# Kernel tuning notes

Measured on AMD Instinct MI355X. Metric: run time of the kernel, lower is better.

Reference implementation:

```python
import jax, jax.numpy as jnp
import numpy as np
from jax import lax

STRIDES = [8, 16, 32, 64, 128]
NUM_CLASSES = 80
PRE_NMS_THRESH = 0.05
PRE_NMS_TOP_N = 1000
NMS_THRESH = 0.6
MAX_DET = 100
IMG_SIZE = 800.0
BBOX_W = (10.0, 10.0, 5.0, 5.0)
SCALE_CLAMP = float(np.log(1000.0 / 16.0))  # Box2BoxTransform clamp


def conv3x3(x, w, b):
    y = lax.conv_general_dilated(x, w, (1, 1), 'SAME',
                                 dimension_numbers=('NCHW', 'OIHW', 'NCHW'))
    return y + b[None, :, None, None]


def conv1x1(x, w, b):
    return jnp.einsum('nchw,kc->nkhw', x, w) + b[None, :, None, None]


def make_anchors(H, W, stride):
    # one square anchor per location, size = 8 * stride (ATSS), offset 0.5
    size = 8.0 * stride
    xs = (jnp.arange(W, dtype=jnp.float32) + 0.5) * stride
    ys = (jnp.arange(H, dtype=jnp.float32) + 0.5) * stride
    cy, cx = jnp.meshgrid(ys, xs, indexing='ij')
    half = size / 2.0
    return jnp.stack([cx - half, cy - half, cx + half, cy + half], -1).reshape(-1, 4)


def decode(deltas, anchors):
    # Box2BoxTransform.apply_deltas with weights (10,10,5,5)
    wx, wy, ww, wh = BBOX_W
    aw = anchors[..., 2] - anchors[..., 0]
    ah = anchors[..., 3] - anchors[..., 1]
    acx = anchors[..., 0] + 0.5 * aw
    acy = anchors[..., 1] + 0.5 * ah
    dx = deltas[..., 0] / wx
    dy = deltas[..., 1] / wy
    dw = jnp.minimum(deltas[..., 2] / ww, SCALE_CLAMP)
    dh = jnp.minimum(deltas[..., 3] / wh, SCALE_CLAMP)
    pcx = dx * aw + acx
    pcy = dy * ah + acy
    pw = jnp.exp(dw) * aw
    ph = jnp.exp(dh) * ah
    boxes = jnp.stack([pcx - 0.5 * pw, pcy - 0.5 * ph,
                       pcx + 0.5 * pw, pcy + 0.5 * ph], -1)
    return jnp.clip(boxes, 0.0, IMG_SIZE)


def iou_one_vs_all(box, boxes):
    x1 = jnp.maximum(box[0], boxes[:, 0])
    y1 = jnp.maximum(box[1], boxes[:, 1])
    x2 = jnp.minimum(box[2], boxes[:, 2])
    y2 = jnp.minimum(box[3], boxes[:, 3])
    inter = jnp.clip(x2 - x1, 0.0) * jnp.clip(y2 - y1, 0.0)
    a1 = (box[2] - box[0]) * (box[3] - box[1])
    a2 = (boxes[:, 2] - boxes[:, 0]) * (boxes[:, 3] - boxes[:, 1])
    return inter / (a1 + a2 - inter + 1e-9)


def nms_single(boxes, scores, classes):
    # class-aware greedy NMS via per-class coordinate offset (ml_nms trick)
    off = classes.astype(boxes.dtype)[:, None] * (2.0 * IMG_SIZE)
    ob = boxes + off

    def step(s, _):
        i = jnp.argmax(s)
        best = s[i]
        iou = iou_one_vs_all(ob[i], ob)
        s = jnp.where(iou > NMS_THRESH, -1.0, s)
        s = s.at[i].set(-1.0)
        return s, (i, best)

    _, (idx, kept) = lax.scan(step, scores, None, length=MAX_DET)
    valid = kept > 0
    out_boxes = jnp.where(valid[:, None], boxes[idx], 0.0)
    out_scores = jnp.where(valid, kept, 0.0)
    out_classes = jnp.where(valid, classes[idx], -1)
    return out_boxes, out_scores, out_classes


def atss_forward(feats, cls_tw, cls_tb, bbox_tw, bbox_tb,
                 wcls, bcls, wbox, bbox_b, wctr, bctr, scales):
    all_boxes, all_scores, all_classes = [], [], []
    for l, x in enumerate(feats):
        c = x
        b = x
        for i in range(cls_tw.shape[0]):  # 4 tower convs
            c = jax.nn.relu(conv3x3(c, cls_tw[i], cls_tb[i]))
            b = jax.nn.relu(conv3x3(b, bbox_tw[i], bbox_tb[i]))
        logits = conv1x1(c, wcls, bcls)               # [N,C,H,W]
        deltas = scales[l] * conv1x1(b, wbox, bbox_b)  # [N,4,H,W]
        ctr = conv1x1(b, wctr, bctr)                   # [N,1,H,W]
        N, C, H, W = logits.shape
        logits = logits.transpose(0, 2, 3, 1).reshape(N, H * W, C)
        deltas = deltas.transpose(0, 2, 3, 1).reshape(N, H * W, 4)
        ctr = ctr.transpose(0, 2, 3, 1).reshape(N, H * W)
        anchors = make_anchors(H, W, STRIDES[l])       # [HW,4]
        # ATSS inference scoring: sigmoid(cls) * sigmoid(centerness)
        s = jax.nn.sigmoid(logits) * jax.nn.sigmoid(ctr)[..., None]
        s = jnp.where(s > PRE_NMS_THRESH, s, 0.0)
        flat = s.reshape(N, -1)                        # [N, HW*C]
        k = min(PRE_NMS_TOP_N, flat.shape[1])
        vals, idx = lax.top_k(flat, k)
        aidx = idx // C
        cidx = idx % C
        d = jnp.take_along_axis(deltas, aidx[:, :, None], axis=1)  # [N,k,4]
        boxes = decode(d, anchors[aidx])
        # final score = sqrt(cls*ctr); safe sqrt to avoid inf grad at 0
        sc = jnp.sqrt(jnp.where(vals > 0, vals, 1.0)) * (vals > 0)
        all_boxes.append(boxes)
        all_scores.append(sc)
        all_classes.append(cidx)
    boxes = jnp.concatenate(all_boxes, 1)
    scores = jnp.concatenate(all_scores, 1)
    classes = jnp.concatenate(all_classes, 1)
    return jax.vmap(nms_single)(boxes, scores, classes)


def setup_inputs() -> dict:
    key = jax.random.key(0)
    ks = jax.random.split(key, 12)
    feats_hw = [(100, 100), (50, 50), (25, 25), (13, 13), (7, 7)]
    N, CIN, CH = 4, 256, 256
    inp = {}
    for i, (h, w) in enumerate(feats_hw):
        inp['p%d' % (i + 3)] = jax.random.normal(ks[i], (N, CIN, h, w), jnp.float32)
    inp['cls_tw'] = jax.random.normal(ks[5], (4, CH, CIN, 3, 3), jnp.float32) * 0.02
    inp['cls_tb'] = jnp.zeros((4, CH), jnp.float32)
    inp['bbox_tw'] = jax.random.normal(ks[6], (4, CH, CIN, 3, 3), jnp.float32) * 0.02
    inp['bbox_tb'] = jnp.zeros((4, CH), jnp.float32)
    inp['wcls'] = jax.random.normal(ks[7], (NUM_CLASSES, CH), jnp.float32) * 0.05
    inp['bcls'] = jnp.zeros((NUM_CLASSES,), jnp.float32)
    inp['wbox'] = jax.random.normal(ks[8], (4, CH), jnp.float32) * 0.05
    inp['bbox_b'] = jnp.zeros((4,), jnp.float32)
    inp['wctr'] = jax.random.normal(ks[9], (1, CH), jnp.float32) * 0.05
    inp['bctr'] = jnp.zeros((1,), jnp.float32)
    inp['scales'] = jnp.ones((5,), jnp.float32)
    return inp


def reference(p3, p4, p5, p6, p7, cls_tw, cls_tb, bbox_tw, bbox_tb,
              wcls, bcls, wbox, bbox_b, wctr, bctr, scales):
    feats = [p3, p4, p5, p6, p7]
    boxes, scores, classes = atss_forward(feats, cls_tw, cls_tb, bbox_tw, bbox_tb,
                                          wcls, bcls, wbox, bbox_b, wctr, bctr, scales)
    return boxes, scores, classes
```

## Files before the change

### kernel.cpp

```cpp
#include <hip/hip_runtime.h>
#include <math.h>

typedef short s8v __attribute__((ext_vector_type(8)));
typedef short s4v __attribute__((ext_vector_type(4)));
typedef float f4v __attribute__((ext_vector_type(4)));
typedef _Float16 h8v __attribute__((ext_vector_type(8)));

__device__ __forceinline__ float sigf(float x) { return 1.f / (1.f + expf(-x)); }
__device__ __forceinline__ float f16f(short v) {
  return (float)__builtin_bit_cast(_Float16, v);
}

#define SCALE_CLAMP 4.135166556742356f
#define IMG_SIZE 800.f
#define PLANE 14482432ull
#define W_SCALE 1024.f
#define A_SCALE 64.f
#define ACC_RESCALE 1.52587890625e-5f

__device__ __forceinline__ void split2(float x, short& h, short& l) {
  _Float16 hf = (_Float16)x;
  _Float16 lf = (_Float16)(x - (float)hf);
  h = __builtin_bit_cast(short, hf);
  l = __builtin_bit_cast(short, lf);
}

struct Geo {
  int tp[6];
  int TXa[5];
  int Ha[5], Wa[5], PWa[5], PHWa[5];
  int phwOff[5];
  int hwOff[5];
  int pb[6];
  int bb[6];
};

__global__ __launch_bounds__(256) void wtrans_k(const float* __restrict__ cls_tw,
                                                const float* __restrict__ bbox_tw,
                                                short* __restrict__ wt)
{
  const int total = 589824;
  for (int u = blockIdx.x * 256 + threadIdx.x; u < total; u += gridDim.x * 256) {
    int layer = u / 73728;
    int r = u - layer * 73728;
    int tap = r / 8192;  r -= tap * 8192;
    int cc  = r / 1024;  r -= cc * 1024;
    int qq  = r / 256;   int ko = r - qq * 256;
    int cibase = cc * 32 + qq * 8;
    const float* src = (layer < 4) ? (cls_tw + (size_t)layer * 589824)
                                   : (bbox_tw + (size_t)(layer - 4) * 589824);
    s8v hv, lv;
#pragma unroll
    for (int e = 0; e < 8; ++e) {
      float x = src[(size_t)ko * 2304 + (size_t)(cibase + e) * 9 + tap] * W_SCALE;
      short h, l; split2(x, h, l);
      hv[e] = h; lv[e] = l;
    }
    size_t dbase = (size_t)layer * 1179648 + (((size_t)tap * 8 + cc) * 4 + qq) * 2048 + (size_t)ko * 8;
    *(s8v*)(wt + dbase) = hv;
    *(s8v*)(wt + dbase + 589824) = lv;
  }
}

__global__ __launch_bounds__(256) void prep_all_k(const float* __restrict__ p3, const float* __restrict__ p4,
                                                  const float* __restrict__ p5, const float* __restrict__ p6,
                                                  const float* __restrict__ p7,
                                                  short* __restrict__ out, Geo g)
{
  __shared__ float tl[64][260];
  int bx = blockIdx.x, t = threadIdx.x, n = blockIdx.y;
  int l = 0; while (l < 4 && bx >= g.pb[l + 1]) ++l;
  const float* in = (l == 0) ? p3 : (l == 1) ? p4 : (l == 2) ? p5 : (l == 3) ? p6 : p7;
  int H = g.Ha[l], W = g.Wa[l], PW = g.PWa[l], PHW = g.PHWa[l], HW = H * W;
  int P0 = (bx - g.pb[l]) * 64;
  const float* inN = in + (size_t)n * HW * 256;
  int sub = t >> 6, pl = t & 63;
  int pos = P0 + pl;
  for (int i = 0; i < 64; ++i) {
    int ci = i * 4 + sub;
    tl[pl][ci] = (pos < HW) ? inN[(size_t)ci * HW + pos] : 0.f;
  }
  __syncthreads();
  int pl2 = t >> 2, cq = (t & 3) * 64;
  int pos2 = P0 + pl2;
  if (pos2 < HW) {
    int y = pos2 / W, x = pos2 - y * W;
    size_t oo = ((size_t)g.phwOff[l] * 4 + (size_t)n * PHW + (size_t)(y + 1) * PW + (x + 1)) * 256 + cq;
#pragma unroll
    for (int grp = 0; grp < 8; ++grp) {
      s8v hv, lv;
#pragma unroll
      for (int e = 0; e < 8; ++e) {
        short h, lo; split2(tl[pl2][cq + grp * 8 + e] * A_SCALE, h, lo);
        hv[e] = h; lv[e] = lo;
      }
      *(s8v*)(out + oo + grp * 8) = hv;
      *(s8v*)(out + PLANE + oo + grp * 8) = lv;
    }
  }
}

#define QS    128
#define PSTR  4096
#define BSTR  8192
__global__ __launch_bounds__(256, 3) void conv_all_k(const short* __restrict__ in0,
                                                     const short* __restrict__ wtL,
                                                     const float* __restrict__ bias,
                                                     short* __restrict__ out0, Geo g)
{
  __shared__ short act_s[2 * BSTR];

  const int t = threadIdx.x;
  const int lane = t & 63, wave = t >> 6;
  const int wcol = wave & 1, wko = wave >> 1;
  const int nT = g.tp[5];
  int bid = blockIdx.x;
  int wgid = (bid & 7) * nT + (bid >> 3);
  const int n = wgid / (2 * nT);
  int r2 = wgid - n * 2 * nT;
  int bx = r2 >> 1;
  const int ko0 = (r2 & 1) * 128;
  int l = 0; while (l < 4 && bx >= g.tp[l + 1]) ++l;
  const int H = g.Ha[l], W = g.Wa[l], PW = g.PWa[l], PHW = g.PHWa[l];
  const int lt = bx - g.tp[l];
  const int TX = g.TXa[l];
  const int ty = lt / TX, tx = lt - ty * TX;
  const int R0 = ty * 4, C0 = tx * 16;
  const size_t bi = ((size_t)g.phwOff[l] * 4 + (size_t)n * PHW) * 256;
  const short* inN = in0 + bi;
  short* outN = out0 + bi;

  const int r = lane & 15, q = lane >> 4;
  const int cb = wcol * 8;
  const short* wlane = wtL + (size_t)q * 2048 + (size_t)(ko0 + wko * 64 + r) * 8;
  const int abase = q * QS + 2 * q + (r >> 3) * 18 + cb + (r & 7);

  int soff[2];
#pragma unroll
  for (int k = 0; k < 2; ++k) {
    int j = t + k * 256;
    int qq = j >> 7, ppos = j & 127;
    int lpos = ppos - 2 * qq;
    if (lpos < 0) lpos = 0;
    if (lpos > 107) lpos = 107;
    int row = lpos / 18, col = lpos - row * 18;
    int prow = R0 + row; if (prow > H + 1) prow = H + 1;
    int pcol = C0 + col; if (pcol > W + 1) pcol = W + 1;
    soff[k] = (prow * PW + pcol) * 256 + qq * 8;
  }

  f4v acc[2][4];
#pragma unroll
  for (int mi = 0; mi < 2; ++mi)
#pragma unroll
    for (int ni = 0; ni < 4; ++ni) { f4v z = {0.f, 0.f, 0.f, 0.f}; acc[mi][ni] = z; }

  auto stage = [&](int cc, int buf) {
#pragma unroll
    for (int k = 0; k < 2; ++k)
#pragma unroll
      for (int p = 0; p < 2; ++p) {
        const short* src = inN + (size_t)p * PLANE + (size_t)(soff[k] + cc * 32);
        short* dst = &act_s[(size_t)buf * BSTR + (size_t)p * PSTR + (size_t)(t + k * 256) * 8];
#if __has_builtin(__builtin_amdgcn_global_load_lds)
        __builtin_amdgcn_global_load_lds((const __attribute__((address_space(1))) void*)src,
                                         (__attribute__((address_space(3))) void*)dst, 16, 0, 0);
#else
        *(s8v*)dst = *(const s8v*)src;
#endif
      }
  };

  auto loadWT = [&](s8v (&w)[2][4], int cc2, int tap2) {
    const short* base = wlane + (size_t)(tap2 * 8 + cc2) * 8192;
#pragma unroll
    for (int p = 0; p < 2; ++p)
#pragma unroll
      for (int k = 0; k < 4; ++k)
        w[p][k] = *(const s8v*)(base + (size_t)p * 589824 + k * 128);
  };

  auto runTap = [&](const s8v (&w)[2][4], int dy, int dx, int buf) {
    s8v afr[2][2];
    const int b0 = buf * BSTR + abase * 8;
    const int d = (dy * 18 + dx) * 8;
#pragma unroll
    for (int mi = 0; mi < 2; ++mi) {
      afr[0][mi] = *(const s8v*)&act_s[b0 + mi * 288 + d];
      afr[1][mi] = *(const s8v*)&act_s[b0 + PSTR + mi * 288 + d];
    }
    const int PA[3] = {0, 0, 1};
    const int PB[3] = {0, 1, 0};
    __builtin_amdgcn_s_setprio(1);
#pragma unroll
    for (int pp = 0; pp < 3; ++pp)
#pragma unroll
      for (int mi = 0; mi < 2; ++mi)
#pragma unroll
        for (int ni = 0; ni < 4; ++ni)
          acc[mi][ni] = __builtin_amdgcn_mfma_f32_16x16x32_f16(
              __builtin_bit_cast(h8v, afr[PA[pp]][mi]),
              __builtin_bit_cast(h8v, w[PB[pp]][ni]),
              acc[mi][ni], 0, 0, 0);
    __builtin_amdgcn_s_setprio(0);
  };

  s8v wA[2][4], wB[2][4];

  auto ccBody = [&](int cc, int buf, s8v (&wF)[2][4], s8v (&wS)[2][4]) {
    if (cc < 7) stage(cc + 1, buf ^ 1);
#pragma unroll
    for (int tap = 0; tap < 9; ++tap) {
      const int dy = tap / 3, dx = tap - dy * 3;
      int ntap = (tap == 8) ? 0 : tap + 1;
      int ncc  = (tap == 8) ? cc + 1 : cc;
      if ((tap & 1) == 0) {
        if (ncc < 8) loadWT(wS, ncc, ntap);
        __builtin_amdgcn_sched_barrier(0);
        runTap(wF, dy, dx, buf);
      } else {
        if (ncc < 8) loadWT(wF, ncc, ntap);
        __builtin_amdgcn_sched_barrier(0);
        runTap(wS, dy, dx, buf);
      }
    }
    __syncthreads();
  };

  stage(0, 0);
  loadWT(wA, 0, 0);
  __syncthreads();

  int cur = 0;
#pragma unroll
  for (int ccp = 0; ccp < 4; ++ccp) {
    ccBody(2 * ccp, cur, wA, wB);
    cur ^= 1;
    ccBody(2 * ccp + 1, cur, wB, wA);
    cur ^= 1;
  }

#pragma unroll
  for (int mi = 0; mi < 2; ++mi) {
#pragma unroll
    for (int ni = 0; ni < 4; ++ni) {
      int ko = ko0 + wko * 64 + ni * 16 + r;
      float bv = bias[ko];
#pragma unroll
      for (int reg = 0; reg < 4; ++reg) {
        int rm = q * 4 + reg;
        int orow = R0 + 2 * mi + (rm >> 3);
        int ocol = C0 + cb + (rm & 7);
        if (orow < H && ocol < W) {
          float real = acc[mi][ni][reg] * ACC_RESCALE + bv;
          float vv = fmaxf(real, 0.f) * A_SCALE;
          short h, lo; split2(vv, h, lo);
          size_t oo = ((size_t)(orow + 1) * PW + (ocol + 1)) * 256 + ko;
          outN[oo] = h; outN[PLANE + oo] = lo;
        }
      }
    }
  }
}

__global__ __launch_bounds__(256) void cls_head_k(const short* __restrict__ act,
                                                  const float* __restrict__ wcls,
                                                  const float* __restrict__ bcls,
                                                  float* __restrict__ score, Geo g)
{
  __shared__ int   p2s[64];
  __shared__ float as_[64][69];
  __shared__ float ws_[64][84];
  const int t = threadIdx.x;
  const int n = blockIdx.y;
  int bx = blockIdx.x;
  int l = 0; while (l < 4 && bx >= g.pb[l + 1]) ++l;
  const int H = g.Ha[l], W = g.Wa[l], PW = g.PWa[l], PHW = g.PHWa[l], HW = H * W;
  const int P0 = (bx - g.pb[l]) * 64;
  if (t < 64) {
    int p = P0 + t; if (p >= HW) p = HW - 1;
    int y = p / W, x = p - y * W;
    p2s[t] = (y + 1) * PW + x + 1;
  }
  __syncthreads();
  float accv[4][5];
#pragma unroll
  for (int i = 0; i < 4; ++i)
#pragma unroll
    for (int j = 0; j < 5; ++j) accv[i][j] = 0.f;

  const short* actN = act + ((size_t)g.phwOff[l] * 4 + (size_t)n * PHW) * 256;
  const int pg = t >> 4, cg = t & 15;
  const float inv = 1.f / A_SCALE;

  for (int c0 = 0; c0 < 256; c0 += 64) {
    for (int i = t; i < 1024; i += 256) {
      int pos = i >> 4, c4 = i & 15;
      size_t o = (size_t)p2s[pos] * 256 + c0 + c4 * 4;
      s4v hv = *(const s4v*)(actN + o);
      s4v lv = *(const s4v*)(actN + PLANE + o);
      float* dst = &as_[pos][c4 * 4];
#pragma unroll
      for (int e = 0; e < 4; ++e) dst[e] = (f16f(hv[e]) + f16f(lv[e])) * inv;
    }
    for (int i = t; i < 1280; i += 256) {
      int c = i >> 4, c4 = i & 15;
      float4 v = *(const float4*)(wcls + (size_t)c * 256 + c0 + c4 * 4);
      ws_[c4 * 4 + 0][c] = v.x; ws_[c4 * 4 + 1][c] = v.y;
      ws_[c4 * 4 + 2][c] = v.z; ws_[c4 * 4 + 3][c] = v.w;
    }
    __syncthreads();
#pragma unroll 8
    for (int ci = 0; ci < 64; ++ci) {
#pragma unroll
      for (int i = 0; i < 4; ++i) {
        float a = as_[pg * 4 + i][ci];
#pragma unroll
        for (int j = 0; j < 5; ++j)
          accv[i][j] = fmaf(a, ws_[ci][cg * 5 + j], accv[i][j]);
      }
    }
    __syncthreads();
  }
  float* sB = score + ((size_t)g.hwOff[l] * 4 + (size_t)n * HW) * 80;
#pragma unroll
  for (int i = 0; i < 4; ++i) {
    int p = P0 + pg * 4 + i;
    if (p >= HW) continue;
#pragma unroll
    for (int j = 0; j < 5; ++j) {
      int c = cg * 5 + j;
      sB[(size_t)p * 80 + c] = sigf(accv[i][j] + bcls[c]);
    }
  }
}

__global__ __launch_bounds__(256) void box_head_k(const short* __restrict__ act,
                                                  const float* __restrict__ wbox,
                                                  const float* __restrict__ bb,
                                                  const float* __restrict__ wctr,
                                                  const float* __restrict__ bc,
                                                  const float* __restrict__ scales,
                                                  float* __restrict__ score,
                                                  float* __restrict__ deltas, Geo g)
{
  int n = blockIdx.y;
  int bx = blockIdx.x;
  int l = 0; while (l < 4 && bx >= g.bb[l + 1]) ++l;
  const int H = g.Ha[l], W = g.Wa[l], PW = g.PWa[l], PHW = g.PHWa[l], HW = H * W;
  int p = (bx - g.bb[l]) * 256 + threadIdx.x;
  if (p >= HW) return;
  int y = p / W, x = p - y * W;
  const short* a = act + ((size_t)g.phwOff[l] * 4 + (size_t)n * PHW + (size_t)(y + 1) * PW + x + 1) * 256;
  const float inv = 1.f / A_SCALE;
  float d0 = 0, d1 = 0, d2 = 0, d3 = 0, ct = 0;
  for (int gI = 0; gI < 32; ++gI) {
    s8v hv = *(const s8v*)(a + gI * 8);
    s8v lv = *(const s8v*)(a + PLANE + gI * 8);
#pragma unroll
    for (int e = 0; e < 8; ++e) {
      float av = (f16f(hv[e]) + f16f(lv[e])) * inv;
      int c = gI * 8 + e;
      d0 = fmaf(av, wbox[c], d0);
      d1 = fmaf(av, wbox[256 + c], d1);
      d2 = fmaf(av, wbox[512 + c], d2);
      d3 = fmaf(av, wbox[768 + c], d3);
      ct = fmaf(av, wctr[c], ct);
    }
  }
  float sl = scales[l];
  float* dd = deltas + ((size_t)g.hwOff[l] * 4 + (size_t)n * HW + p) * 4;
  dd[0] = sl * (d0 + bb[0]); dd[1] = sl * (d1 + bb[1]);
  dd[2] = sl * (d2 + bb[2]); dd[3] = sl * (d3 + bb[3]);
  float sct = sigf(ct + bc[0]);
  float* sp = score + ((size_t)g.hwOff[l] * 4 + (size_t)n * HW + p) * 80;
#pragma unroll
  for (int i = 0; i < 20; ++i) {
    float4 v = ((float4*)sp)[i];
    v.x *= sct; v.y *= sct; v.z *= sct; v.w *= sct;
    v.x = (v.x > 0.05f) ? v.x : 0.f;
    v.y = (v.y > 0.05f) ? v.y : 0.f;
    v.z = (v.z > 0.05f) ? v.z : 0.f;
    v.w = (v.w > 0.05f) ? v.w : 0.f;
    ((float4*)sp)[i] = v;
  }
}

__global__ __launch_bounds__(256) void hist_k(const float* __restrict__ score,
                                              const unsigned* __restrict__ thr,
                                              unsigned* __restrict__ hist, int phase, Geo g)
{
  const int grp = blockIdx.y;
  const int l = grp >> 2, n = grp & 3;
  const int HW = g.Ha[l] * g.Wa[l];
  const int M = HW * 80;
  const float* s = score + ((size_t)g.hwOff[l] * 4 + (size_t)n * HW) * 80;
  unsigned* h = hist + grp * 2048;
  const unsigned* tr = thr + grp * 8;
  __shared__ unsigned lh[2048];
  for (int i = threadIdx.x; i < 2048; i += 256) lh[i] = 0u;
  __syncthreads();
  unsigned B1 = 0, pref = 0;
  if (phase == 1) B1 = tr[0];
  if (phase == 2) pref = (tr[0] << 11) | tr[1];
  for (int idx = blockIdx.x * 256 + threadIdx.x; idx < M; idx += gridDim.x * 256) {
    float v = s[idx];
    if (v > 0.f) {
      unsigned b = __float_as_uint(v);
      if (phase == 0) atomicAdd(&lh[b >> 20], 1u);
      else if (phase == 1) { if ((b >> 20) == B1) atomicAdd(&lh[(b >> 9) & 0x7FFu], 1u); }
      else { if ((b >> 9) == pref) atomicAdd(&lh[b & 0x1FFu], 1u); }
    }
  }
  __syncthreads();
  for (int i = threadIdx.x; i < 2048; i += 256) { unsigned v = lh[i]; if (v) atomicAdd(&h[i], v); }
}

__global__ __launch_bounds__(256) void scan_k(unsigned* __restrict__ hist,
                                              unsigned* __restrict__ thr, int phase)
{
  const int grp = blockIdx.x, t = threadIdx.x;
  unsigned* h  = hist + grp * 2048;
  unsigned* tr = thr + grp * 8;
  const int nb = (phase == 2) ? 512 : 2048;
  const int PB = nb / 256;
  unsigned target = 1000u;
  bool dead = false;
  if (phase >= 1) {
    target = 1000u - tr[2];
    if (tr[0] == 0xFFFFFFFFu) dead = true;
    if (phase == 2 && tr[1] == 0xFFFFFFFFu) dead = true;
  }
  __shared__ unsigned ps[256];
  __shared__ unsigned s_tot;
  const int hi = nb - t * PB;
  unsigned lsum = 0;
  for (int k = 0; k < PB; ++k) lsum += h[hi - 1 - k];
  ps[t] = lsum;
  __syncthreads();
  if (t == 0) {
    unsigned cum = 0;
    for (int i = 0; i < 256; ++i) { unsigned tmp = ps[i]; ps[i] = cum; cum += tmp; }
    s_tot = cum;
  }
  __syncthreads();
  unsigned exc = ps[t], tot = s_tot;
  if (!dead && tot >= target) {
    if (exc < target && exc + lsum >= target) {
      unsigned cum = exc; int bf = 0; unsigned above = 0;
      for (int k = 0; k < PB; ++k) {
        int bidx = hi - 1 - k;
        unsigned c = h[bidx];
        if (cum < target && cum + c >= target) { bf = bidx; above = cum; }
        cum += c;
      }
      if (phase == 0)      { tr[0] = (unsigned)bf; tr[2] = above; }
      else if (phase == 1) { tr[1] = (unsigned)bf; tr[2] = tr[2] + above; }
      else {
        unsigned T = (tr[0] << 20) | (tr[1] << 9) | (unsigned)bf;
        tr[3] = T; tr[4] = target - above;
      }
    }
  } else if (t == 0) {
    if (phase == 0)      { tr[0] = 0xFFFFFFFFu; tr[2] = 0u; }
    else if (phase == 1) { tr[1] = 0xFFFFFFFFu; }
    else                 { tr[3] = 0u; tr[4] = 0u; }
  }
  if (phase == 2 && t == 0) { tr[5] = 0u; tr[6] = 0u; }
}

__global__ __launch_bounds__(256) void select_k(const float* __restrict__ score,
                                                const float* __restrict__ deltas,
                                                unsigned* __restrict__ thr,
                                                float* __restrict__ cbox, float* __restrict__ csc,
                                                float* __restrict__ ccls, float* __restrict__ cgid,
                                                Geo g)
{
  const int grp = blockIdx.y;
  const int l = grp >> 2, n = grp & 3;
  const int W = g.Wa[l];
  const int HW = g.Ha[l] * W;
  const int M = HW * 80;
  const float stride_ = (float)(8 << l);
  const float* s = score + ((size_t)g.hwOff[l] * 4 + (size_t)n * HW) * 80;
  const float* dBase = deltas + ((size_t)g.hwOff[l] * 4 + (size_t)n * HW) * 4;
  unsigned* tr = thr + grp * 8;
  const unsigned T = tr[3], need = tr[4];
  for (int idx = blockIdx.x * 256 + threadIdx.x; idx < M; idx += gridDim.x * 256) {
    float v = s[idx];
    if (!(v > 0.f)) continue;
    unsigned b = __float_as_uint(v);
    int slot = -1;
    if (b > T) slot = (int)atomicAdd(&tr[5], 1u);
    else if (b == T) {
      unsigned e = atomicAdd(&tr[6], 1u);
      if (e < need) slot = (int)(1000u - need + e);
    }
    if (slot < 0) continue;
    int p = idx / 80, c = idx - p * 80;
    int y = p / W, x = p - y * W;
    const float* d = dBase + (size_t)p * 4;
    float sz  = 8.f * stride_;
    float acx = ((float)x + 0.5f) * stride_;
    float acy = ((float)y + 0.5f) * stride_;
    float dx = d[0] / 10.f, dy = d[1] / 10.f;
    float dw = fminf(d[2] / 5.f, SCALE_CLAMP);
    float dh = fminf(d[3] / 5.f, SCALE_CLAMP);
    float pcx = dx * sz + acx;
    float pcy = dy * sz + acy;
    float pw = expf(dw) * sz;
    float ph = expf(dh) * sz;
    float x1 = pcx - 0.5f * pw, y1_ = pcy - 0.5f * ph;
    float x2 = pcx + 0.5f * pw, y2_ = pcy + 0.5f * ph;
    x1  = fminf(fmaxf(x1, 0.f),  IMG_SIZE);
    y1_ = fminf(fmaxf(y1_, 0.f), IMG_SIZE);
    x2  = fminf(fmaxf(x2, 0.f),  IMG_SIZE);
    y2_ = fminf(fmaxf(y2_, 0.f), IMG_SIZE);
    int cslot = n * 5000 + l * 1000 + slot;
    ((float4*)cbox)[cslot] = make_float4(x1, y1_, x2, y2_);
    csc[cslot]  = sqrtf(v);
    ccls[cslot] = (float)c;
    cgid[cslot] = (float)(((unsigned)l << 20) | (unsigned)idx);
  }
}

__global__ __launch_bounds__(256) void nms_bucket_k(const float* __restrict__ cbox,
                                                    const float* __restrict__ csc,
                                                    const float* __restrict__ ccls,
                                                    const float* __restrict__ cgid,
                                                    float4* __restrict__ bbox2,
                                                    unsigned long long* __restrict__ bkey2,
                                                    int* __restrict__ coff)
{
  __shared__ unsigned cnt[80];
  __shared__ unsigned off_s[81];
  const int n = blockIdx.x, t = threadIdx.x;
  for (int i = t; i < 80; i += 256) cnt[i] = 0u;
  __syncthreads();
  for (int i = t; i < 5000; i += 256) {
    float s = csc[n * 5000 + i];
    if (s > 0.f) atomicAdd(&cnt[(int)ccls[n * 5000 + i]], 1u);
  }
  __syncthreads();
  if (t == 0) {
    unsigned c = 0;
    for (int k = 0; k < 80; ++k) { off_s[k] = c; c += cnt[k]; }
    off_s[80] = c;
  }
  __syncthreads();
  for (int i = t; i < 81; i += 256) coff[n * 81 + i] = (int)off_s[i];
  for (int i = t; i < 80; i += 256) cnt[i] = 0u;
  __syncthreads();
  for (int i = t; i < 5000; i += 256) {
    float s = csc[n * 5000 + i];
    if (s > 0.f) {
      int c = (int)ccls[n * 5000 + i];
      unsigned p = atomicAdd(&cnt[c], 1u);
      int dst = n * 5000 + (int)off_s[c] + (int)p;
      bbox2[dst] = ((const float4*)cbox)[n * 5000 + i];
      unsigned long long sb = (unsigned long long)__float_as_uint(s);
      unsigned gid = (unsigned)cgid[n * 5000 + i];
      bkey2[dst] = (sb << 24) | (unsigned long long)(0xFFFFFFu - gid);
    }
  }
}

#define NCAP 1536
__global__ __launch_bounds__(64) void nms_class_k(const float4* __restrict__ bbox2,
                                                  unsigned long long* __restrict__ bkey2,
                                                  const int* __restrict__ coff,
                                                  float4* __restrict__ kbox,
                                                  unsigned long long* __restrict__ kkey,
                                                  int* __restrict__ kcnt)
{
  __shared__ unsigned long long key_s[NCAP];
  __shared__ unsigned long long sk_s[NCAP];
  __shared__ float4 sb_s[NCAP];
  __shared__ unsigned char af_s[NCAP + 64];
  const int cls = blockIdx.x, n = blockIdx.y, t = threadIdx.x;
  const int lo = coff[n * 81 + cls], hi = coff[n * 81 + cls + 1];
  const int c = hi - lo;
  const int base = n * 5000 + lo;
  const int outB = (n * 80 + cls) * 100;
  int kept = 0;
  if (c > 0 && c <= NCAP) {
    const int nch = (c + 63) >> 6;
    for (int i = t; i < nch * 64; i += 64) af_s[i] = 0;
    for (int i = t; i < c; i += 64) key_s[i] = bkey2[base + i];
    __syncthreads();
    for (int i = t; i < c; i += 64) {
      unsigned long long ki = key_s[i];
      int rk = 0;
      for (int m = 0; m < c; ++m) rk += (key_s[m] > ki) ? 1 : 0;
      sk_s[rk] = ki;
      sb_s[rk] = bbox2[base + i];
      af_s[rk] = 1;
    }
    __syncthreads();
    int p = -1;
    while (kept < 100) {
      int np = -1;
      int j0 = (p + 1) >> 6;
      for (int j = j0; j < nch; ++j) {
        int pos = j * 64 + t;
        unsigned long long w = __ballot(af_s[pos] != 0);
        if (j == j0) { int sh = (p + 1) & 63; if (sh) w &= (~0ull) << sh; }
        if (w) { np = j * 64 + (int)__builtin_ctzll(w); break; }
      }
      if (np < 0) break;
      p = np;
      float4 wb = sb_s[p];
      if (t == 0) { kbox[outB + kept] = wb; kkey[outB + kept] = sk_s[p]; }
      ++kept;
      float a1 = (wb.z - wb.x) * (wb.w - wb.y);
      for (int i = p + t; i < c; i += 64) {
        if (!af_s[i]) continue;
        float4 b = sb_s[i];
        float xx1 = fmaxf(wb.x, b.x), yy1 = fmaxf(wb.y, b.y);
        float xx2 = fminf(wb.z, b.z), yy2 = fminf(wb.w, b.w);
        float inter = fmaxf(xx2 - xx1, 0.f) * fmaxf(yy2 - yy1, 0.f);
        float a2 = (b.z - b.x) * (b.w - b.y);
        if (inter / (a1 + a2 - inter + 1e-9f) > 0.6f) af_s[i] = 0;
      }
      __syncthreads();
    }
  } else if (c > NCAP) {
    while (kept < 100) {
      unsigned long long best = 0ull; int bi = 0;
      for (int i = t; i < c; i += 64) {
        unsigned long long k = bkey2[base + i];
        if (k > best) { best = k; bi = i; }
      }
#pragma unroll
      for (int o = 32; o; o >>= 1) {
        unsigned long long ok = __shfl_xor(best, o);
        int oi = __shfl_xor(bi, o);
        if (ok > best) { best = ok; bi = oi; }
      }
      if (best == 0ull) break;
      float4 wb = bbox2[base + bi];
      if (t == 0) { kbox[outB + kept] = wb; kkey[outB + kept] = best; }
      ++kept;
      float a1 = (wb.z - wb.x) * (wb.w - wb.y);
      for (int i = t; i < c; i += 64) {
        unsigned long long k = bkey2[base + i];
        if (!k) continue;
        float4 b = bbox2[base + i];
        float xx1 = fmaxf(wb.x, b.x), yy1 = fmaxf(wb.y, b.y);
        float xx2 = fminf(wb.z, b.z), yy2 = fminf(wb.w, b.w);
        float inter = fmaxf(xx2 - xx1, 0.f) * fmaxf(yy2 - yy1, 0.f);
        float a2 = (b.z - b.x) * (b.w - b.y);
        if (inter / (a1 + a2 - inter + 1e-9f) > 0.6f) bkey2[base + i] = 0ull;
      }
      __syncthreads();
    }
  }
  if (t == 0) kcnt[n * 80 + cls] = kept;
}

__global__ __launch_bounds__(64) void nms_merge_k(const float4* __restrict__ kbox,
                                                  const unsigned long long* __restrict__ kkey,
                                                  const int* __restrict__ kcnt,
                                                  float* __restrict__ outp)
{
  __shared__ unsigned long long lk[8000];
  __shared__ int head[80];
  __shared__ int cnts[80];
  const int n = blockIdx.x, t = threadIdx.x;
  for (int i = t; i < 80; i += 64) { head[i] = 0; cnts[i] = kcnt[n * 80 + i]; }
  for (int i = t; i < 8000; i += 64) lk[i] = kkey[n * 8000 + i];
  __syncthreads();
  for (int it = 0; it < 100; ++it) {
    unsigned long long best = 0ull; int bc = 0;
    for (int cls = t; cls < 80; cls += 64) {
      int h = head[cls];
      if (h < cnts[cls]) {
        unsigned long long k = lk[cls * 100 + h];
        if (k > best) { best = k; bc = cls; }
      }
    }
#pragma unroll
    for (int o = 32; o; o >>= 1) {
      unsigned long long ok = __shfl_xor(best, o);
      int oc = __shfl_xor(bc, o);
      if (ok > best) { best = ok; bc = oc; }
    }
    if (t == 0) {
      int basei = n * 100 + it;
      if (best != 0ull) {
        int idx = (n * 80 + bc) * 100 + head[bc];
        float4 b = kbox[idx];
        outp[basei * 4 + 0] = b.x; outp[basei * 4 + 1] = b.y;
        outp[basei * 4 + 2] = b.z; outp[basei * 4 + 3] = b.w;
        outp[1600 + basei] = __uint_as_float((unsigned)(best >> 24));
        outp[2000 + basei] = (float)bc;
        head[bc] = head[bc] + 1;
      } else {
        outp[basei * 4 + 0] = 0.f; outp[basei * 4 + 1] = 0.f;
        outp[basei * 4 + 2] = 0.f; outp[basei * 4 + 3] = 0.f;
        outp[1600 + basei] = 0.f;
        outp[2000 + basei] = -1.f;
      }
    }
    __syncthreads();
  }
}

extern "C" void kernel_launch(void* const* d_in, const int* in_sizes, int n_in,
                              void* d_out, int out_size, void* d_ws, size_t ws_size,
                              hipStream_t stream)
{
  (void)in_sizes; (void)n_in; (void)out_size; (void)ws_size;
  const float* p3 = (const float*)d_in[0];
  const float* p4 = (const float*)d_in[1];
  const float* p5 = (const float*)d_in[2];
  const float* p6 = (const float*)d_in[3];
  const float* p7 = (const float*)d_in[4];
  const float* cls_tw  = (const float*)d_in[5];
  const float* cls_tb  = (const float*)d_in[6];
  const float* bbox_tw = (const float*)d_in[7];
  const float* bbox_tb = (const float*)d_in[8];
  const float* wcls    = (const float*)d_in[9];
  const float* bcls    = (const float*)d_in[10];
  const float* wbox    = (const float*)d_in[11];
  const float* bbox_b  = (const float*)d_in[12];
  const float* wctr    = (const float*)d_in[13];
  const float* bctr    = (const float*)d_in[14];
  const float* scales  = (const float*)d_in[15];
  float* out = (float*)d_out;

  Geo G;
  const int Hs[5] = {100, 50, 25, 13, 7};
  {
    int tpre = 0, ppre = 0, bpre = 0, phw = 0, hw = 0;
    for (int l = 0; l < 5; ++l) {
      int H = Hs[l], W = Hs[l];
      G.Ha[l] = H; G.Wa[l] = W; G.PWa[l] = W + 2; G.PHWa[l] = (H + 2) * (W + 2);
      G.TXa[l] = (W + 15) / 16;
      int TY = (H + 3) / 4;
      G.tp[l] = tpre;  tpre += G.TXa[l] * TY;
      G.pb[l] = ppre;  ppre += (H * W + 63) / 64;
      G.bb[l] = bpre;  bpre += (H * W + 255) / 256;
      G.phwOff[l] = phw; phw += G.PHWa[l];
      G.hwOff[l]  = hw;  hw  += H * W;
    }
    G.tp[5] = tpre; G.pb[5] = ppre; G.bb[5] = bpre;
  }
  const int nTiles = G.tp[5];
  const int nPrep  = G.pb[5];
  const int nBoxB  = G.bb[5];
  const int sumHW = 13343;
  const size_t scoreBytes  = (size_t)sumHW * 4 * 80 * 4;
  const size_t deltasBytes = (size_t)sumHW * 4 * 4 * 4;

  char* ws = (char*)d_ws;
  size_t off = 0;
  auto alloc = [&](size_t bytes) -> void* {
    off = (off + 255) & ~(size_t)255;
    void* p = ws + off; off += bytes; return p;
  };
  const size_t bufBytes = 2ull * PLANE * 2;

  short* wt     = (short*)alloc((size_t)8 * 2 * 589824 * 2);
  float* cbox   = (float*)alloc(4ull * 5000 * 4 * 4);
  float* csc    = (float*)alloc(4ull * 5000 * 4);
  float* ccls   = (float*)alloc(4ull * 5000 * 4);
  float* cgid   = (float*)alloc(4ull * 5000 * 4);
  unsigned* hist = (unsigned*)alloc(20ull * 2048 * 4);
  unsigned* thr  = (unsigned*)alloc(20ull * 8 * 4);
  float4* bbox2 = (float4*)alloc(4ull * 5000 * 16);
  unsigned long long* bkey2 = (unsigned long long*)alloc(4ull * 5000 * 8);
  int* coff     = (int*)alloc(4ull * 81 * 4);
  float4* kbox  = (float4*)alloc(320ull * 100 * 16);
  unsigned long long* kkey = (unsigned long long*)alloc(320ull * 100 * 8);
  int* kcnt     = (int*)alloc(320ull * 4);
  short* C = (short*)alloc(bufBytes);
  short* A = (short*)alloc(bufBytes);
  short* B = (short*)alloc(bufBytes);
  float* score  = (float*)alloc(scoreBytes);
  float* deltas = (float*)alloc(deltasBytes);

  hipMemsetAsync(csc,  0, 4ull * 5000 * 4, stream);
  hipMemsetAsync(ccls, 0, 4ull * 5000 * 4, stream);
  hipMemsetAsync(cgid, 0, 4ull * 5000 * 4, stream);
  hipMemsetAsync(thr,  0, 20ull * 8 * 4, stream);
  hipMemsetAsync(C, 0, bufBytes, stream);
  hipMemsetAsync(A, 0, bufBytes, stream);
  hipMemsetAsync(B, 0, bufBytes, stream);

  wtrans_k<<<1024, 256, 0, stream>>>(cls_tw, bbox_tw, wt);

  const size_t LSTRIDE = 2ull * 589824;
  dim3 cg(8 * nTiles);

  prep_all_k<<<dim3(nPrep, 4), 256, 0, stream>>>(p3, p4, p5, p6, p7, C, G);
  conv_all_k<<<cg, 256, 0, stream>>>(C, wt + 0 * LSTRIDE, cls_tb + 0 * 256, A, G);
  conv_all_k<<<cg, 256, 0, stream>>>(A, wt + 1 * LSTRIDE, cls_tb + 1 * 256, B, G);
  conv_all_k<<<cg, 256, 0, stream>>>(B, wt + 2 * LSTRIDE, cls_tb + 2 * 256, A, G);
  conv_all_k<<<cg, 256, 0, stream>>>(A, wt + 3 * LSTRIDE, cls_tb + 3 * 256, B, G);
  cls_head_k<<<dim3(nPrep, 4), 256, 0, stream>>>(B, wcls, bcls, score, G);
  conv_all_k<<<cg, 256, 0, stream>>>(C, wt + 4 * LSTRIDE, bbox_tb + 0 * 256, A, G);
  conv_all_k<<<cg, 256, 0, stream>>>(A, wt + 5 * LSTRIDE, bbox_tb + 1 * 256, C, G);
  conv_all_k<<<cg, 256, 0, stream>>>(C, wt + 6 * LSTRIDE, bbox_tb + 2 * 256, A, G);
  conv_all_k<<<cg, 256, 0, stream>>>(A, wt + 7 * LSTRIDE, bbox_tb + 3 * 256, C, G);
  box_head_k<<<dim3(nBoxB, 4), 256, 0, stream>>>(C, wbox, bbox_b, wctr, bctr, scales,
                                                 score, deltas, G);

  const int hb = 196;
  for (int phase = 0; phase < 3; ++phase) {
    hipMemsetAsync(hist, 0, 20ull * 2048 * 4, stream);
    hist_k<<<dim3(hb, 20), 256, 0, stream>>>(score, thr, hist, phase, G);
    scan_k<<<20, 256, 0, stream>>>(hist, thr, phase);
  }
  select_k<<<dim3(hb, 20), 256, 0, stream>>>(score, deltas, thr, cbox, csc, ccls, cgid, G);

  nms_bucket_k<<<4, 256, 0, stream>>>(cbox, csc, ccls, cgid, bbox2, bkey2, coff);
  nms_class_k<<<dim3(80, 4), 64, 0, stream>>>(bbox2, bkey2, coff, kbox, kkey, kcnt);
  nms_merge_k<<<4, 64, 0, stream>>>(kbox, kkey, kcnt, out);
}
```

Baseline: 2.177 ms.

## Run cls and bbox tower convs in one launch per layer

Merges the classification and box tower convolutions of each layer into a single launch with twice the grid, choosing the input, weights, bias and output per block by a tower index. This halves the number of conv launches and gives each launch more blocks, so more of the GPU is busy and tail effects shrink. It needs a fourth activation buffer and reuses one buffer for scores and deltas, with a fallback to the old sequence when the workspace is too small. Launch bounds also go from 3 to 4 waves per SIMD, which may limit registers and cause spills.

```diff
diff --git a/kernel.cpp b/kernel.cpp
--- a/kernel.cpp
+++ b/kernel.cpp
@@ -103,10 +103,14 @@
 #define QS    128
 #define PSTR  4096
 #define BSTR  8192
-__global__ __launch_bounds__(256, 3) void conv_all_k(const short* __restrict__ in0,
-                                                     const short* __restrict__ wtL,
-                                                     const float* __restrict__ bias,
-                                                     short* __restrict__ out0, Geo g)
+__global__ __launch_bounds__(256, 4) void conv_all_k(const short* __restrict__ in0,
+                                                     const short* __restrict__ in1,
+                                                     const short* __restrict__ wt0,
+                                                     const short* __restrict__ wt1,
+                                                     const float* __restrict__ bias0,
+                                                     const float* __restrict__ bias1,
+                                                     short* __restrict__ out0,
+                                                     short* __restrict__ out1, Geo g)
 {
   __shared__ short act_s[2 * BSTR];
 
@@ -114,12 +118,19 @@
   const int lane = t & 63, wave = t >> 6;
   const int wcol = wave & 1, wko = wave >> 1;
   const int nT = g.tp[5];
+  const int nhalf = 2 * nT;
   int bid = blockIdx.x;
-  int wgid = (bid & 7) * nT + (bid >> 3);
-  const int n = wgid / (2 * nT);
-  int r2 = wgid - n * 2 * nT;
+  int wgid = (bid & 7) * nhalf + (bid >> 3);
+  const int it = wgid / nhalf;
+  const int tower = it >> 2;
+  const int n = it & 3;
+  int r2 = wgid - it * nhalf;
   int bx = r2 >> 1;
   const int ko0 = (r2 & 1) * 128;
+  const short* in   = tower ? in1 : in0;
+  const short* wtL  = tower ? wt1 : wt0;
+  const float* bias = tower ? bias1 : bias0;
+  short* out        = tower ? out1 : out0;
   int l = 0; while (l < 4 && bx >= g.tp[l + 1]) ++l;
   const int H = g.Ha[l], W = g.Wa[l], PW = g.PWa[l], PHW = g.PHWa[l];
   const int lt = bx - g.tp[l];
@@ -127,8 +138,8 @@
   const int ty = lt / TX, tx = lt - ty * TX;
   const int R0 = ty * 4, C0 = tx * 16;
   const size_t bi = ((size_t)g.phwOff[l] * 4 + (size_t)n * PHW) * 256;
-  const short* inN = in0 + bi;
-  short* outN = out0 + bi;
+  const short* inN = in + bi;
+  short* outN = out + bi;
 
   const int r = lane & 15, q = lane >> 4;
   const int cb = wcol * 8;
@@ -710,7 +721,7 @@
                               void* d_out, int out_size, void* d_ws, size_t ws_size,
                               hipStream_t stream)
 {
-  (void)in_sizes; (void)n_in; (void)out_size; (void)ws_size;
+  (void)in_sizes; (void)n_in; (void)out_size;
   const float* p3 = (const float*)d_in[0];
   const float* p4 = (const float*)d_in[1];
   const float* p5 = (const float*)d_in[2];
@@ -774,37 +785,77 @@
   float4* kbox  = (float4*)alloc(320ull * 100 * 16);
   unsigned long long* kkey = (unsigned long long*)alloc(320ull * 100 * 8);
   int* kcnt     = (int*)alloc(320ull * 4);
-  short* C = (short*)alloc(bufBytes);
-  short* A = (short*)alloc(bufBytes);
-  short* B = (short*)alloc(bufBytes);
-  float* score  = (float*)alloc(scoreBytes);
-  float* deltas = (float*)alloc(deltasBytes);
+  const size_t fixedEnd = (off + 255) & ~(size_t)255;
+  const bool fused = (ws_size >= fixedEnd + 4 * (bufBytes + 256) + 8192);
 
   hipMemsetAsync(csc,  0, 4ull * 5000 * 4, stream);
   hipMemsetAsync(ccls, 0, 4ull * 5000 * 4, stream);
   hipMemsetAsync(cgid, 0, 4ull * 5000 * 4, stream);
   hipMemsetAsync(thr,  0, 20ull * 8 * 4, stream);
-  hipMemsetAsync(C, 0, bufBytes, stream);
-  hipMemsetAsync(A, 0, bufBytes, stream);
-  hipMemsetAsync(B, 0, bufBytes, stream);
 
   wtrans_k<<<1024, 256, 0, stream>>>(cls_tw, bbox_tw, wt);
 
   const size_t LSTRIDE = 2ull * 589824;
-  dim3 cg(8 * nTiles);
-
-  prep_all_k<<<dim3(nPrep, 4), 256, 0, stream>>>(p3, p4, p5, p6, p7, C, G);
-  conv_all_k<<<cg, 256, 0, stream>>>(C, wt + 0 * LSTRIDE, cls_tb + 0 * 256, A, G);
-  conv_all_k<<<cg, 256, 0, stream>>>(A, wt + 1 * LSTRIDE, cls_tb + 1 * 256, B, G);
-  conv_all_k<<<cg, 256, 0, stream>>>(B, wt + 2 * LSTRIDE, cls_tb + 2 * 256, A, G);
-  conv_all_k<<<cg, 256, 0, stream>>>(A, wt + 3 * LSTRIDE, cls_tb + 3 * 256, B, G);
-  cls_head_k<<<dim3(nPrep, 4), 256, 0, stream>>>(B, wcls, bcls, score, G);
-  conv_all_k<<<cg, 256, 0, stream>>>(C, wt + 4 * LSTRIDE, bbox_tb + 0 * 256, A, G);
-  conv_all_k<<<cg, 256, 0, stream>>>(A, wt + 5 * LSTRIDE, bbox_tb + 1 * 256, C, G);
-  conv_all_k<<<cg, 256, 0, stream>>>(C, wt + 6 * LSTRIDE, bbox_tb + 2 * 256, A, G);
-  conv_all_k<<<cg, 256, 0, stream>>>(A, wt + 7 * LSTRIDE, bbox_tb + 3 * 256, C, G);
-  box_head_k<<<dim3(nBoxB, 4), 256, 0, stream>>>(C, wbox, bbox_b, wctr, bctr, scales,
-                                                 score, deltas, G);
+  float* score;
+  float* deltas;
+
+  if (fused) {
+    short* C = (short*)alloc(bufBytes);
+    short* A = (short*)alloc(bufBytes);
+    short* B = (short*)alloc(bufBytes);
+    short* D = (short*)alloc(bufBytes);
+    score  = (float*)A;
+    deltas = (float*)((char*)A + ((scoreBytes + 255) & ~(size_t)255));
+    hipMemsetAsync(C, 0, bufBytes, stream);
+    hipMemsetAsync(A, 0, bufBytes, stream);
+    hipMemsetAsync(B, 0, bufBytes, stream);
+    hipMemsetAsync(D, 0, bufBytes, stream);
+
+    prep_all_k<<<dim3(nPrep, 4), 256, 0, stream>>>(p3, p4, p5, p6, p7, C, G);
+    dim3 cg(16 * nTiles);
+    conv_all_k<<<cg, 256, 0, stream>>>(C, C, wt + 0 * LSTRIDE, wt + 4 * LSTRIDE,
+                                       cls_tb + 0 * 256, bbox_tb + 0 * 256, A, B, G);
+    conv_all_k<<<cg, 256, 0, stream>>>(A, B, wt + 1 * LSTRIDE, wt + 5 * LSTRIDE,
+                                       cls_tb + 1 * 256, bbox_tb + 1 * 256, C, D, G);
+    conv_all_k<<<cg, 256, 0, stream>>>(C, D, wt + 2 * LSTRIDE, wt + 6 * LSTRIDE,
+                                       cls_tb + 2 * 256, bbox_tb + 2 * 256, A, B, G);
+    conv_all_k<<<cg, 256, 0, stream>>>(A, B, wt + 3 * LSTRIDE, wt + 7 * LSTRIDE,
+                                       cls_tb + 3 * 256, bbox_tb + 3 * 256, C, D, G);
+    cls_head_k<<<dim3(nPrep, 4), 256, 0, stream>>>(C, wcls, bcls, score, G);
+    box_head_k<<<dim3(nBoxB, 4), 256, 0, stream>>>(D, wbox, bbox_b, wctr, bctr, scales,
+                                                   score, deltas, G);
+  } else {
+    short* C = (short*)alloc(bufBytes);
+    short* A = (short*)alloc(bufBytes);
+    short* B = (short*)alloc(bufBytes);
+    score  = (float*)alloc(scoreBytes);
+    deltas = (float*)alloc(deltasBytes);
+    hipMemsetAsync(C, 0, bufBytes, stream);
+    hipMemsetAsync(A, 0, bufBytes, stream);
+    hipMemsetAsync(B, 0, bufBytes, stream);
+
+    prep_all_k<<<dim3(nPrep, 4), 256, 0, stream>>>(p3, p4, p5, p6, p7, C, G);
+    dim3 cg(8 * nTiles);
+    conv_all_k<<<cg, 256, 0, stream>>>(C, C, wt + 0 * LSTRIDE, wt + 0 * LSTRIDE,
+                                       cls_tb + 0 * 256, cls_tb + 0 * 256, A, A, G);
+    conv_all_k<<<cg, 256, 0, stream>>>(A, A, wt + 1 * LSTRIDE, wt + 1 * LSTRIDE,
+                                       cls_tb + 1 * 256, cls_tb + 1 * 256, B, B, G);
+    conv_all_k<<<cg, 256, 0, stream>>>(B, B, wt + 2 * LSTRIDE, wt + 2 * LSTRIDE,
+                                       cls_tb + 2 * 256, cls_tb + 2 * 256, A, A, G);
+    conv_all_k<<<cg, 256, 0, stream>>>(A, A, wt + 3 * LSTRIDE, wt + 3 * LSTRIDE,
+                                       cls_tb + 3 * 256, cls_tb + 3 * 256, B, B, G);
+    cls_head_k<<<dim3(nPrep, 4), 256, 0, stream>>>(B, wcls, bcls, score, G);
+    conv_all_k<<<cg, 256, 0, stream>>>(C, C, wt + 4 * LSTRIDE, wt + 4 * LSTRIDE,
+                                       bbox_tb + 0 * 256, bbox_tb + 0 * 256, A, A, G);
+    conv_all_k<<<cg, 256, 0, stream>>>(A, A, wt + 5 * LSTRIDE, wt + 5 * LSTRIDE,
+                                       bbox_tb + 1 * 256, bbox_tb + 1 * 256, C, C, G);
+    conv_all_k<<<cg, 256, 0, stream>>>(C, C, wt + 6 * LSTRIDE, wt + 6 * LSTRIDE,
+                                       bbox_tb + 2 * 256, bbox_tb + 2 * 256, A, A, G);
+    conv_all_k<<<cg, 256, 0, stream>>>(A, A, wt + 7 * LSTRIDE, wt + 7 * LSTRIDE,
+                                       bbox_tb + 3 * 256, bbox_tb + 3 * 256, C, C, G);
+    box_head_k<<<dim3(nBoxB, 4), 256, 0, stream>>>(C, wbox, bbox_b, wctr, bctr, scales,
+                                                   score, deltas, G);
+  }
 
   const int hb = 196;
   for (int phase = 0; phase < 3; ++phase) {
```

Result: slower. 2.279 ms (+4.6%).
